# Kernel optimization log

Measured on AMD Instinct MI355X. Metric: run time of the kernel, lower is better.

## Reference

```python
import jax, jax.numpy as jnp
import numpy as np

B, T, F, D, HD = 16, 512, 16, 256, 256


def _init(k, shape, fan_in):
    return (jax.random.uniform(k, shape, minval=-1.0, maxval=1.0) / np.sqrt(fan_in)).astype(jnp.float32)


def setup_inputs() -> dict:
    key = jax.random.key(0)
    ks = jax.random.split(key, 16)
    return {
        "x": jax.random.normal(ks[0], (B, T, F), dtype=jnp.float32),
        # per-variable encoder params, batched over F (Linear(1,D) + GRN(D,HD,D))
        "w1": _init(ks[1], (F, D), 1), "b1": _init(ks[2], (F, D), 1),
        "fc1_w": _init(ks[3], (F, D, HD), D), "fc1_b": _init(ks[4], (F, HD), D),
        "fc2_w": _init(ks[5], (F, HD, D), HD), "fc2_b": _init(ks[6], (F, D), HD),
        "glu_w": _init(ks[7], (F, D, 2 * D), D), "glu_b": _init(ks[8], (F, 2 * D), D),
        "ln_g": jnp.ones((F, D), jnp.float32), "ln_b": jnp.zeros((F, D), jnp.float32),
        # weight GRN(F, HD, F); skip is Identity since d_in == d_out
        "wg_fc1_w": _init(ks[9], (F, HD), F), "wg_fc1_b": _init(ks[10], (HD,), F),
        "wg_fc2_w": _init(ks[11], (HD, F), HD), "wg_fc2_b": _init(ks[12], (F,), HD),
        "wg_glu_w": _init(ks[13], (F, 2 * F), F), "wg_glu_b": _init(ks[14], (2 * F,), F),
        "wg_ln_g": jnp.ones((F,), jnp.float32), "wg_ln_b": jnp.zeros((F,), jnp.float32),
    }


def _layernorm(x, g, b, eps=1e-5):
    m = jnp.mean(x, axis=-1, keepdims=True)
    v = jnp.var(x, axis=-1, keepdims=True)
    return (x - m) * jax.lax.rsqrt(v + eps) * g + b


def reference(x, w1, b1, fc1_w, fc1_b, fc2_w, fc2_b, glu_w, glu_b, ln_g, ln_b,
              wg_fc1_w, wg_fc1_b, wg_fc2_w, wg_fc2_b, wg_glu_w, wg_glu_b,
              wg_ln_g, wg_ln_b):
    # --- per-variable towers, batched over F (dropout is identity at eval) ---
    h0 = jax.nn.relu(x[..., None] * w1 + b1)                       # [B,T,F,D]
    y = jax.nn.elu(jnp.einsum('btfd,fdh->btfh', h0, fc1_w) + fc1_b)
    y = jnp.einsum('btfh,fhd->btfd', y, fc2_w) + fc2_b
    g = jnp.einsum('btfd,fde->btfe', y, glu_w) + glu_b             # [B,T,F,2D]
    a, gate = jnp.split(g, 2, axis=-1)
    H = _layernorm(h0 + a * jax.nn.sigmoid(gate), ln_g, ln_b)      # [B,T,F,D]
    # --- variable-weight GRN (time_distributed=True) ---
    yw = jax.nn.elu(x @ wg_fc1_w + wg_fc1_b)
    yw = yw @ wg_fc2_w + wg_fc2_b
    gw = x @ jnp.zeros((F, 0), x.dtype) if False else yw @ wg_glu_w + wg_glu_b
    aw, gatew = jnp.split(gw, 2, axis=-1)
    w = _layernorm(x + aw * jax.nn.sigmoid(gatew), wg_ln_g, wg_ln_b)
    w = jax.nn.softmax(w, axis=-1)                                 # [B,T,F]
    z = jnp.einsum('btfd,btf->btd', H, w)                          # [B,T,D]
    return z, w
```

## Files before the change

### kernel.cpp

```cpp
#include <hip/hip_runtime.h>
#include <hip/hip_bf16.h>

#define NBT 8192
#define NF  16
#define ND  256
#define NH  256
#define N2D 512

typedef short bf16x8 __attribute__((ext_vector_type(8)));
typedef float f32x4 __attribute__((ext_vector_type(4)));
typedef unsigned short u16x8 __attribute__((ext_vector_type(8)));

__device__ __forceinline__ float bf2f(unsigned short u) {
  return __uint_as_float(((unsigned)u) << 16);
}
__device__ __forceinline__ unsigned short f2bf(float f) {
  unsigned u = __float_as_uint(f);
  return (unsigned short)((u + 0x7FFFu + ((u >> 16) & 1u)) >> 16);
}

#define GLOAD16(src, dst)                                                     \
  __builtin_amdgcn_global_load_lds(                                           \
      (const __attribute__((address_space(1))) unsigned int*)(src),           \
      (__attribute__((address_space(3))) unsigned int*)(dst), 16, 0, 0)

__global__ __launch_bounds__(256) void wgrn_kernel(
    const float* __restrict__ x, const float* __restrict__ fw1,
    const float* __restrict__ fb1, const float* __restrict__ fw2,
    const float* __restrict__ fb2, const float* __restrict__ gwt,
    const float* __restrict__ gbt, const float* __restrict__ lng,
    const float* __restrict__ lnb, float* __restrict__ wout) {
  __shared__ float w1t[256 * 16];
  __shared__ float w2s[256 * 16];
  const int tid = threadIdx.x;
  for (int i = tid; i < 4096; i += 256) {
    int ff = i >> 8, j = i & 255;
    w1t[j * 16 + ff] = fw1[i];
    w2s[i] = fw2[i];
  }
  __syncthreads();
  const int sub  = tid & 7;
  const int rowi = tid >> 3;
  const int bt   = blockIdx.x * 32 + rowi;
  float xr[16];
#pragma unroll
  for (int i = 0; i < 4; ++i)
    *(float4*)&xr[i * 4] = *(const float4*)(x + (size_t)bt * 16 + i * 4);
  float acc2[16];
#pragma unroll
  for (int q = 0; q < 16; ++q) acc2[q] = 0.f;
  for (int j = sub; j < 256; j += 8) {
    float h = fb1[j];
    const float* wr = &w1t[j * 16];
#pragma unroll
    for (int q = 0; q < 16; ++q) h = fmaf(xr[q], wr[q], h);
    h = h > 0.f ? h : expm1f(h);
    const float* w2r = &w2s[j * 16];
#pragma unroll
    for (int q = 0; q < 16; ++q) acc2[q] = fmaf(h, w2r[q], acc2[q]);
  }
#pragma unroll
  for (int off = 1; off < 8; off <<= 1) {
#pragma unroll
    for (int q = 0; q < 16; ++q) acc2[q] += __shfl_xor(acc2[q], off);
  }
#pragma unroll
  for (int q = 0; q < 16; ++q) acc2[q] += fb2[q];
  float gw[32];
#pragma unroll
  for (int k = 0; k < 32; ++k) {
    float s = gbt[k];
#pragma unroll
    for (int q = 0; q < 16; ++q) s = fmaf(acc2[q], gwt[q * 32 + k], s);
    gw[k] = s;
  }
  float v[16];
  float mean = 0.f;
#pragma unroll
  for (int q = 0; q < 16; ++q) {
    float sg = 1.f / (1.f + __expf(-gw[16 + q]));
    v[q] = fmaf(gw[q], sg, xr[q]);
    mean += v[q];
  }
  mean *= (1.f / 16.f);
  float var = 0.f;
#pragma unroll
  for (int q = 0; q < 16; ++q) { float d = v[q] - mean; var = fmaf(d, d, var); }
  var *= (1.f / 16.f);
  float rstd = rsqrtf(var + 1e-5f);
  float mx = -1e30f;
#pragma unroll
  for (int q = 0; q < 16; ++q) {
    v[q] = (v[q] - mean) * rstd * lng[q] + lnb[q];
    mx = fmaxf(mx, v[q]);
  }
  float se = 0.f;
#pragma unroll
  for (int q = 0; q < 16; ++q) { v[q] = __expf(v[q] - mx); se += v[q]; }
  float inv = 1.f / se;
  if (sub == 0) {
#pragma unroll
    for (int i = 0; i < 4; ++i) {
      float4 o = { v[i*4+0]*inv, v[i*4+1]*inv, v[i*4+2]*inv, v[i*4+3]*inv };
      *(float4*)(wout + (size_t)bt * 16 + i * 4) = o;
    }
  }
}

__global__ void transpose_all(const float* __restrict__ fc1_w,
                              const float* __restrict__ fc2_w,
                              const float* __restrict__ glu_w,
                              unsigned short* __restrict__ fc1t,
                              unsigned short* __restrict__ fc2t,
                              unsigned short* __restrict__ glut) {
  __shared__ float tile[32][33];
  const int which = blockIdx.z >> 4;
  const int f     = blockIdx.z & 15;
  const float* src;
  unsigned short* dst;
  int K, N, bx = blockIdx.x;
  if (which == 0)      { src = fc1_w; dst = fc1t; K = ND; N = NH; }
  else if (which == 1) { src = fc2_w; dst = fc2t; K = NH; N = ND; }
  else                 { src = glu_w; dst = glut; K = ND; N = N2D;
                         bx += (which == 3) ? 8 : 0; }
  if (bx * 32 >= N) return;
  const float* s = src + (size_t)f * K * N;
  unsigned short* d = dst + (size_t)f * K * N;
  const int k0 = blockIdx.y * 32, n0 = bx * 32;
  const int tx = threadIdx.x, ty = threadIdx.y;
#pragma unroll
  for (int i = 0; i < 32; i += 8)
    tile[ty + i][tx] = s[(size_t)(k0 + ty + i) * N + n0 + tx];
  __syncthreads();
#pragma unroll
  for (int i = 0; i < 32; i += 8)
    d[(size_t)(n0 + ty + i) * K + k0 + tx] = f2bf(tile[tx][ty + i]);
}

__global__ __launch_bounds__(256, 4) void g1_kernel(
    const float* __restrict__ x, const float* __restrict__ w1,
    const float* __restrict__ b1, const unsigned short* __restrict__ fc1t,
    const float* __restrict__ fc1_b, unsigned short* __restrict__ y1) {
  __shared__ __align__(16) char arena[34816];
  __shared__ float xw[128];
  unsigned short* abuf = (unsigned short*)arena;
  unsigned short* bbuf = (unsigned short*)(arena + 17408);
  unsigned short* cbuf = (unsigned short*)arena;
  const int tid = threadIdx.x, lane = tid & 63, wid = tid >> 6;
  const int rl = lane & 15, kc = lane >> 4;
  int hb = blockIdx.x + 2 * (blockIdx.y + 64 * blockIdx.z);
  int L  = (hb & 7) * 256 + (hb >> 3);
  const int f = L >> 7, m0 = ((L >> 1) & 63) * 128, n0 = (L & 1) * 128;
  const unsigned short* Bf = fc1t + (size_t)f * NH * ND;
  const float* w1f = w1 + f * ND;
  const float* b1f = b1 + f * ND;
  if (tid < 128) xw[tid] = x[(size_t)(m0 + tid) * NF + f];
  const int wm = (wid >> 1) * 64, wn = (wid & 1) * 64;

  f32x4 acc[4][4];
#pragma unroll
  for (int m = 0; m < 4; ++m)
#pragma unroll
    for (int n = 0; n < 4; ++n) acc[m][n] = (f32x4){0.f, 0.f, 0.f, 0.f};

  for (int kt = 0; kt < ND; kt += 64) {
    __syncthreads();
#pragma unroll
    for (int i = 0; i < 4; ++i) {
      int s = tid + 256 * i;
      int row = s >> 3, sl = s & 7;
      const unsigned short* gb =
          Bf + (size_t)(n0 + row) * ND + kt + ((sl ^ (row & 7)) << 3);
      GLOAD16(gb, (char*)bbuf + (wid * 64 + 256 * i) * 16);
    }
#pragma unroll
    for (int i = 0; i < 4; ++i) {
      int vi = tid + 256 * i;
      int row = vi >> 3, c8 = vi & 7, c = kt + c8 * 8;
      float xv = xw[row];
      float4 wa = *(const float4*)(w1f + c);
      float4 wb = *(const float4*)(w1f + c + 4);
      float4 ba = *(const float4*)(b1f + c);
      float4 bb = *(const float4*)(b1f + c + 4);
      u16x8 o;
      o[0] = f2bf(fmaxf(fmaf(xv, wa.x, ba.x), 0.f));
      o[1] = f2bf(fmaxf(fmaf(xv, wa.y, ba.y), 0.f));
      o[2] = f2bf(fmaxf(fmaf(xv, wa.z, ba.z), 0.f));
      o[3] = f2bf(fmaxf(fmaf(xv, wa.w, ba.w), 0.f));
      o[4] = f2bf(fmaxf(fmaf(xv, wb.x, bb.x), 0.f));
      o[5] = f2bf(fmaxf(fmaf(xv, wb.y, bb.y), 0.f));
      o[6] = f2bf(fmaxf(fmaf(xv, wb.z, bb.z), 0.f));
      o[7] = f2bf(fmaxf(fmaf(xv, wb.w, bb.w), 0.f));
      *(u16x8*)(abuf + row * 68 + c8 * 8) = o;
    }
    __syncthreads();
#pragma unroll
    for (int kk = 0; kk < 2; ++kk) {
      bf16x8 av[4], bv[4];
      int s = kk * 4 + kc;
#pragma unroll
      for (int m = 0; m < 4; ++m) {
        int r = wm + m * 16 + rl;
        av[m] = *(const bf16x8*)(abuf + r * 68 + s * 8);
      }
#pragma unroll
      for (int n = 0; n < 4; ++n) {
        int rr = wn + n * 16 + rl;
        int ps = s ^ (rr & 7);
        bv[n] = *(const bf16x8*)((const char*)bbuf + rr * 128 + ps * 16);
      }
#pragma unroll
      for (int m = 0; m < 4; ++m)
#pragma unroll
        for (int n = 0; n < 4; ++n)
          acc[m][n] = __builtin_amdgcn_mfma_f32_16x16x32_bf16(av[m], bv[n],
                                                              acc[m][n], 0, 0, 0);
    }
  }

  __syncthreads();
  const int rq = lane >> 4;
#pragma unroll
  for (int n = 0; n < 4; ++n) {
    int cl = wn + n * 16 + rl;
    float bvv = fc1_b[f * NH + n0 + cl];
#pragma unroll
    for (int m = 0; m < 4; ++m) {
#pragma unroll
      for (int j = 0; j < 4; ++j) {
        int r = wm + m * 16 + rq * 4 + j;
        float v = acc[m][n][j] + bvv;
        v = v > 0.f ? v : expm1f(v);
        cbuf[r * 136 + cl] = f2bf(v);
      }
    }
  }
  __syncthreads();
#pragma unroll
  for (int v = 0; v < 8; ++v) {
    int row = (tid >> 4) + v * 16, chunk = tid & 15;
    u16x8 val = *(const u16x8*)(cbuf + row * 136 + chunk * 8);
    *(u16x8*)(y1 + ((size_t)f * NBT + m0 + row) * NH + n0 + chunk * 8) = val;
  }
}

__global__ __launch_bounds__(512, 4) void g2_kernel(
    const unsigned short* __restrict__ y1,
    const unsigned short* __restrict__ fc2t, const float* __restrict__ fc2_b,
    unsigned short* __restrict__ y2) {
  __shared__ __align__(16) char arena[49152];
  unsigned short* abuf = (unsigned short*)arena;
  unsigned short* bbuf = (unsigned short*)(arena + 16384);
  unsigned short* cbuf = (unsigned short*)arena;
  const int tid = threadIdx.x, lane = tid & 63, wid = tid >> 6;
  const int rl = lane & 15, kc = lane >> 4;
  int hb = blockIdx.x + 64 * blockIdx.y;
  int L  = (hb & 7) * 128 + (hb >> 3);
  const int f = L >> 6, m0 = (L & 63) * 128;
  const unsigned short* Af = y1 + (size_t)f * NBT * NH;
  const unsigned short* Bf = fc2t + (size_t)f * ND * NH;
  const int wm = (wid >> 2) * 64, wn = (wid & 3) * 64;

  f32x4 acc[4][4];
#pragma unroll
  for (int m = 0; m < 4; ++m)
#pragma unroll
    for (int n = 0; n < 4; ++n) acc[m][n] = (f32x4){0.f, 0.f, 0.f, 0.f};

  for (int kt = 0; kt < NH; kt += 64) {
    __syncthreads();
#pragma unroll
    for (int i = 0; i < 2; ++i) {
      int s = tid + 512 * i;
      int row = s >> 3, sl = s & 7;
      const unsigned short* ga =
          Af + (size_t)(m0 + row) * NH + kt + ((sl ^ (row & 7)) << 3);
      GLOAD16(ga, (char*)abuf + (wid * 64 + 512 * i) * 16);
    }
#pragma unroll
    for (int i = 0; i < 4; ++i) {
      int s = tid + 512 * i;
      int row = s >> 3, sl = s & 7;
      const unsigned short* gb =
          Bf + (size_t)row * NH + kt + ((sl ^ (row & 7)) << 3);
      GLOAD16(gb, (char*)bbuf + (wid * 64 + 512 * i) * 16);
    }
    __syncthreads();
#pragma unroll
    for (int kk = 0; kk < 2; ++kk) {
      bf16x8 av[4], bv[4];
      int s = kk * 4 + kc;
#pragma unroll
      for (int m = 0; m < 4; ++m) {
        int r = wm + m * 16 + rl;
        int ps = s ^ (r & 7);
        av[m] = *(const bf16x8*)((const char*)abuf + r * 128 + ps * 16);
      }
#pragma unroll
      for (int n = 0; n < 4; ++n) {
        int rr = wn + n * 16 + rl;
        int ps = s ^ (rr & 7);
        bv[n] = *(const bf16x8*)((const char*)bbuf + rr * 128 + ps * 16);
      }
#pragma unroll
      for (int m = 0; m < 4; ++m)
#pragma unroll
        for (int n = 0; n < 4; ++n)
          acc[m][n] = __builtin_amdgcn_mfma_f32_16x16x32_bf16(av[m], bv[n],
                                                              acc[m][n], 0, 0, 0);
    }
  }

  __syncthreads();
  const int rq = lane >> 4;
  const int hsel = (wid & 3) >> 1;
#pragma unroll
  for (int h = 0; h < 2; ++h) {
    if (h) __syncthreads();
    if (hsel == h) {
#pragma unroll
      for (int n = 0; n < 4; ++n) {
        int c = wn + n * 16 + rl;
        int cl = c - h * 128;
        float bvv = fc2_b[f * ND + c];
#pragma unroll
        for (int m = 0; m < 4; ++m) {
#pragma unroll
          for (int j = 0; j < 4; ++j) {
            int r = wm + m * 16 + rq * 4 + j;
            cbuf[r * 136 + cl] = f2bf(acc[m][n][j] + bvv);
          }
        }
      }
    }
    __syncthreads();
#pragma unroll
    for (int v = 0; v < 4; ++v) {
      int row = (tid >> 4) + v * 32, chunk = tid & 15;
      u16x8 val = *(const u16x8*)(cbuf + row * 136 + chunk * 8);
      *(u16x8*)(y2 + ((size_t)f * NBT + m0 + row) * ND + h * 128 + chunk * 8) =
          val;
    }
  }
}

__global__ __launch_bounds__(512, 4) void g3_kernel(
    const unsigned short* __restrict__ y2,
    const unsigned short* __restrict__ glut, const float* __restrict__ glu_b,
    const float* __restrict__ x, const float* __restrict__ w1,
    const float* __restrict__ b1, const float* __restrict__ ln_g,
    const float* __restrict__ ln_b, unsigned short* __restrict__ H) {
  __shared__ __align__(16) char arena[73728];
  __shared__ float xw[64];
  __shared__ float2 sums[8][64];
  __shared__ float2 sums2[64];
  unsigned short* abuf = (unsigned short*)arena;
  unsigned short* bbuf = (unsigned short*)(arena + 8192);
  unsigned short* vbuf = (unsigned short*)arena;

  const int tid = threadIdx.x, lane = tid & 63, wid = tid >> 6;
  const int rl = lane & 15, rq = lane >> 4;
  int hb = blockIdx.x + 128 * blockIdx.y;
  int L  = (hb & 7) * 256 + (hb >> 3);
  const int f = L >> 7, m0 = (L & 127) * 64;
  const unsigned short* Af = y2 + (size_t)f * NBT * ND;
  const unsigned short* Bf = glut + (size_t)f * ND * N2D;
  const float* w1f = w1 + f * ND;
  const float* b1f = b1 + f * ND;
  const int colb = wid * 32;
  if (tid < 64) xw[tid] = x[(size_t)(m0 + tid) * NF + f];

  f32x4 acc[4][4];
#pragma unroll
  for (int m = 0; m < 4; ++m)
#pragma unroll
    for (int n = 0; n < 4; ++n) acc[m][n] = (f32x4){0.f, 0.f, 0.f, 0.f};

  for (int kt = 0; kt < ND; kt += 64) {
    __syncthreads();
    {
      int s = tid;
      int row = s >> 3, sl = s & 7;
      const unsigned short* ga =
          Af + (size_t)(m0 + row) * ND + kt + ((sl ^ (row & 7)) << 3);
      GLOAD16(ga, (char*)abuf + (wid * 64) * 16);
    }
#pragma unroll
    for (int i = 0; i < 8; ++i) {
      int s = tid + 512 * i;
      int row = s >> 3, sl = s & 7;
      const unsigned short* gb =
          Bf + (size_t)row * ND + kt + ((sl ^ (row & 7)) << 3);
      GLOAD16(gb, (char*)bbuf + (wid * 64 + 512 * i) * 16);
    }
    __syncthreads();
#pragma unroll
    for (int kk = 0; kk < 2; ++kk) {
      bf16x8 av[4], bv[4];
      int s = kk * 4 + rq;
#pragma unroll
      for (int m = 0; m < 4; ++m) {
        int r = m * 16 + rl;
        int ps = s ^ (r & 7);
        av[m] = *(const bf16x8*)((const char*)abuf + r * 128 + ps * 16);
      }
#pragma unroll
      for (int n = 0; n < 4; ++n) {
        int rr = (n < 2) ? (colb + n * 16 + rl)
                         : (256 + colb + (n - 2) * 16 + rl);
        int ps = s ^ (rr & 7);
        bv[n] = *(const bf16x8*)((const char*)bbuf + rr * 128 + ps * 16);
      }
#pragma unroll
      for (int m = 0; m < 4; ++m)
#pragma unroll
        for (int n = 0; n < 4; ++n)
          acc[m][n] = __builtin_amdgcn_mfma_f32_16x16x32_bf16(av[m], bv[n],
                                                              acc[m][n], 0, 0, 0);
    }
  }

#pragma unroll
  for (int n = 0; n < 2; ++n) {
    int cA = colb + n * 16 + rl;
    float ab_ = glu_b[f * N2D + cA];
    float gb_ = glu_b[f * N2D + 256 + cA];
    float w1c = w1f[cA], b1c = b1f[cA];
#pragma unroll
    for (int m = 0; m < 4; ++m) {
#pragma unroll
      for (int j = 0; j < 4; ++j) {
        int r = m * 16 + rq * 4 + j;
        float a = acc[m][n][j] + ab_;
        float g = acc[m][n + 2][j] + gb_;
        float sg = 1.f / (1.f + __expf(-g));
        float h0 = fmaxf(fmaf(xw[r], w1c, b1c), 0.f);
        acc[m][n][j] = fmaf(a, sg, h0);
      }
    }
  }
#pragma unroll
  for (int m = 0; m < 4; ++m) {
#pragma unroll
    for (int j = 0; j < 4; ++j) {
      float s = acc[m][0][j] + acc[m][1][j];
      float q = fmaf(acc[m][0][j], acc[m][0][j],
                     acc[m][1][j] * acc[m][1][j]);
#pragma unroll
      for (int off = 1; off < 16; off <<= 1) {
        s += __shfl_xor(s, off);
        q += __shfl_xor(q, off);
      }
      if (rl == 0) sums[wid][m * 16 + rq * 4 + j] = make_float2(s, q);
    }
  }
  __syncthreads();
  if (tid < 64) {
    float tot = 0.f, tot2 = 0.f;
#pragma unroll
    for (int wv = 0; wv < 8; ++wv) {
      float2 p = sums[wv][tid];
      tot += p.x;
      tot2 += p.y;
    }
    float mean = tot * (1.f / 256.f);
    float var  = tot2 * (1.f / 256.f) - mean * mean;
    sums2[tid] = make_float2(mean, rsqrtf(var + 1e-5f));
  }
  __syncthreads();
#pragma unroll
  for (int n = 0; n < 2; ++n) {
    int cA = colb + n * 16 + rl;
    float lg = ln_g[f * ND + cA], lb = ln_b[f * ND + cA];
#pragma unroll
    for (int m = 0; m < 4; ++m) {
#pragma unroll
      for (int j = 0; j < 4; ++j) {
        int r = m * 16 + rq * 4 + j;
        float2 mr = sums2[r];
        vbuf[r * 264 + cA] = f2bf(fmaf((acc[m][n][j] - mr.x) * mr.y, lg, lb));
      }
    }
  }
  __syncthreads();
  {
    int row = tid >> 3, chunk = tid & 7;
    unsigned short* Hrow = H + ((size_t)f * NBT + m0 + row) * ND;
#pragma unroll
    for (int v = 0; v < 4; ++v) {
      u16x8 val = *(const u16x8*)(vbuf + row * 264 + chunk * 8 + v * 64);
      *(u16x8*)(Hrow + chunk * 8 + v * 64) = val;
    }
  }
}

__global__ __launch_bounds__(256) void combine_kernel(
    const unsigned short* __restrict__ H, const float* __restrict__ w,
    float* __restrict__ z) {
  int idx = blockIdx.x * 256 + threadIdx.x;
  int bt = idx >> 5;
  int d  = (idx & 31) << 3;
  float a[8];
#pragma unroll
  for (int j = 0; j < 8; ++j) a[j] = 0.f;
#pragma unroll
  for (int f = 0; f < 16; ++f) {
    u16x8 hv = *(const u16x8*)(H + ((size_t)f * NBT + bt) * ND + d);
    float wvv = w[bt * 16 + f];
#pragma unroll
    for (int j = 0; j < 8; ++j) a[j] = fmaf(bf2f(hv[j]), wvv, a[j]);
  }
  float4 o0 = {a[0], a[1], a[2], a[3]};
  float4 o1 = {a[4], a[5], a[6], a[7]};
  *(float4*)(z + (size_t)bt * ND + d)     = o0;
  *(float4*)(z + (size_t)bt * ND + d + 4) = o1;
}

extern "C" void kernel_launch(void* const* d_in, const int* in_sizes, int n_in,
                              void* d_out, int out_size, void* d_ws,
                              size_t ws_size, hipStream_t stream) {
  const float* x        = (const float*)d_in[0];
  const float* w1       = (const float*)d_in[1];
  const float* b1       = (const float*)d_in[2];
  const float* fc1_w    = (const float*)d_in[3];
  const float* fc1_b    = (const float*)d_in[4];
  const float* fc2_w    = (const float*)d_in[5];
  const float* fc2_b    = (const float*)d_in[6];
  const float* glu_w    = (const float*)d_in[7];
  const float* glu_b    = (const float*)d_in[8];
  const float* ln_g     = (const float*)d_in[9];
  const float* ln_b     = (const float*)d_in[10];
  const float* wg_fc1_w = (const float*)d_in[11];
  const float* wg_fc1_b = (const float*)d_in[12];
  const float* wg_fc2_w = (const float*)d_in[13];
  const float* wg_fc2_b = (const float*)d_in[14];
  const float* wg_glu_w = (const float*)d_in[15];
  const float* wg_glu_b = (const float*)d_in[16];
  const float* wg_ln_g  = (const float*)d_in[17];
  const float* wg_ln_b  = (const float*)d_in[18];

  char* ws = (char*)d_ws;
  unsigned short* fc1t = (unsigned short*)ws;
  unsigned short* fc2t = fc1t + (size_t)NF * NH * ND;
  unsigned short* glut = fc2t + (size_t)NF * ND * NH;
  unsigned short* y1   = (unsigned short*)(ws + (8ull << 20));
  unsigned short* y2   = (unsigned short*)(ws + (72ull << 20));
  unsigned short* Hbuf = (unsigned short*)(ws + (136ull << 20));

  float* zout = (float*)d_out;
  float* wout = zout + (size_t)NBT * ND;

  wgrn_kernel<<<256, 256, 0, stream>>>(x, wg_fc1_w, wg_fc1_b, wg_fc2_w,
                                       wg_fc2_b, wg_glu_w, wg_glu_b, wg_ln_g,
                                       wg_ln_b, wout);
  transpose_all<<<dim3(16, 8, 64), dim3(32, 8), 0, stream>>>(
      fc1_w, fc2_w, glu_w, fc1t, fc2t, glut);

  g1_kernel<<<dim3(NH / 128, NBT / 128, NF), 256, 0, stream>>>(
      x, w1, b1, fc1t, fc1_b, y1);
  g2_kernel<<<dim3(NBT / 128, NF), 512, 0, stream>>>(y1, fc2t, fc2_b, y2);
  g3_kernel<<<dim3(NBT / 64, NF), 512, 0, stream>>>(y2, glut, glu_b, x, w1, b1,
                                                    ln_g, ln_b, Hbuf);
  combine_kernel<<<(NBT * ND / 8) / 256, 256, 0, stream>>>(Hbuf, wout, zout);

  (void)in_sizes; (void)n_in; (void)out_size; (void)ws_size;
}
```

Measured before the change: 227.0 us.

## Fuse fc1 and fc2 GEMMs into one kernel keeping intermediate in LDS

Merges the first two per-variable GEMMs into a single kernel. Each block computes a 64-row tile of h0, runs fc1 with ELU into shared memory, then runs fc2 from that shared tile, so the y1 intermediate never goes to global memory. This removes a 64 MB bf16 write plus its read-back and one kernel launch. In exchange the tiles are smaller (64 rows, 32 columns per wave), with fewer MFMAs per B-tile load, a larger LDS footprint and lower occupancy per CU.

Measured after the change: 195.5 us, median of 2. 13.9% less time.

```diff
diff --git a/kernel.cpp b/kernel.cpp
--- a/kernel.cpp
+++ b/kernel.cpp
@@ -137,210 +137,164 @@
     d[(size_t)(n0 + ty + i) * K + k0 + tx] = f2bf(tile[tx][ty + i]);
 }
 
-__global__ __launch_bounds__(256, 4) void g1_kernel(
+__global__ __launch_bounds__(512, 2) void g12_kernel(
     const float* __restrict__ x, const float* __restrict__ w1,
     const float* __restrict__ b1, const unsigned short* __restrict__ fc1t,
-    const float* __restrict__ fc1_b, unsigned short* __restrict__ y1) {
-  __shared__ __align__(16) char arena[34816];
-  __shared__ float xw[128];
-  unsigned short* abuf = (unsigned short*)arena;
-  unsigned short* bbuf = (unsigned short*)(arena + 17408);
-  unsigned short* cbuf = (unsigned short*)arena;
+    const float* __restrict__ fc1_b, const unsigned short* __restrict__ fc2t,
+    const float* __restrict__ fc2_b, unsigned short* __restrict__ y2) {
+  __shared__ __align__(16) unsigned short hbuf[64 * 264];
+  __shared__ __align__(16) unsigned short bstg[256 * 64];
+  __shared__ float xw[64];
   const int tid = threadIdx.x, lane = tid & 63, wid = tid >> 6;
   const int rl = lane & 15, kc = lane >> 4;
-  int hb = blockIdx.x + 2 * (blockIdx.y + 64 * blockIdx.z);
+  int hb = blockIdx.x + 128 * blockIdx.y;
   int L  = (hb & 7) * 256 + (hb >> 3);
-  const int f = L >> 7, m0 = ((L >> 1) & 63) * 128, n0 = (L & 1) * 128;
-  const unsigned short* Bf = fc1t + (size_t)f * NH * ND;
+  const int f = L >> 7, m0 = (L & 127) * 64;
+  const unsigned short* B1 = fc1t + (size_t)f * NH * ND;
+  const unsigned short* B2 = fc2t + (size_t)f * ND * NH;
   const float* w1f = w1 + f * ND;
   const float* b1f = b1 + f * ND;
-  if (tid < 128) xw[tid] = x[(size_t)(m0 + tid) * NF + f];
-  const int wm = (wid >> 1) * 64, wn = (wid & 1) * 64;
-
-  f32x4 acc[4][4];
+  const int wn = wid * 32;
+
+  if (tid < 64) xw[tid] = x[(size_t)(m0 + tid) * NF + f];
+  __syncthreads();
+
+#pragma unroll
+  for (int i = 0; i < 4; ++i) {
+    int j = tid + 512 * i;
+    int row = j >> 5, c = (j & 31) * 8;
+    float xv = xw[row];
+    float4 wa = *(const float4*)(w1f + c);
+    float4 wb = *(const float4*)(w1f + c + 4);
+    float4 ba = *(const float4*)(b1f + c);
+    float4 bb = *(const float4*)(b1f + c + 4);
+    u16x8 o;
+    o[0] = f2bf(fmaxf(fmaf(xv, wa.x, ba.x), 0.f));
+    o[1] = f2bf(fmaxf(fmaf(xv, wa.y, ba.y), 0.f));
+    o[2] = f2bf(fmaxf(fmaf(xv, wa.z, ba.z), 0.f));
+    o[3] = f2bf(fmaxf(fmaf(xv, wa.w, ba.w), 0.f));
+    o[4] = f2bf(fmaxf(fmaf(xv, wb.x, bb.x), 0.f));
+    o[5] = f2bf(fmaxf(fmaf(xv, wb.y, bb.y), 0.f));
+    o[6] = f2bf(fmaxf(fmaf(xv, wb.z, bb.z), 0.f));
+    o[7] = f2bf(fmaxf(fmaf(xv, wb.w, bb.w), 0.f));
+    *(u16x8*)(hbuf + row * 264 + c) = o;
+  }
+  __syncthreads();
+
+  f32x4 acc[4][2];
 #pragma unroll
   for (int m = 0; m < 4; ++m)
 #pragma unroll
-    for (int n = 0; n < 4; ++n) acc[m][n] = (f32x4){0.f, 0.f, 0.f, 0.f};
+    for (int n = 0; n < 2; ++n) acc[m][n] = (f32x4){0.f, 0.f, 0.f, 0.f};
 
   for (int kt = 0; kt < ND; kt += 64) {
-    __syncthreads();
-#pragma unroll
-    for (int i = 0; i < 4; ++i) {
-      int s = tid + 256 * i;
-      int row = s >> 3, sl = s & 7;
-      const unsigned short* gb =
-          Bf + (size_t)(n0 + row) * ND + kt + ((sl ^ (row & 7)) << 3);
-      GLOAD16(gb, (char*)bbuf + (wid * 64 + 256 * i) * 16);
-    }
-#pragma unroll
-    for (int i = 0; i < 4; ++i) {
-      int vi = tid + 256 * i;
-      int row = vi >> 3, c8 = vi & 7, c = kt + c8 * 8;
-      float xv = xw[row];
-      float4 wa = *(const float4*)(w1f + c);
-      float4 wb = *(const float4*)(w1f + c + 4);
-      float4 ba = *(const float4*)(b1f + c);
-      float4 bb = *(const float4*)(b1f + c + 4);
-      u16x8 o;
-      o[0] = f2bf(fmaxf(fmaf(xv, wa.x, ba.x), 0.f));
-      o[1] = f2bf(fmaxf(fmaf(xv, wa.y, ba.y), 0.f));
-      o[2] = f2bf(fmaxf(fmaf(xv, wa.z, ba.z), 0.f));
-      o[3] = f2bf(fmaxf(fmaf(xv, wa.w, ba.w), 0.f));
-      o[4] = f2bf(fmaxf(fmaf(xv, wb.x, bb.x), 0.f));
-      o[5] = f2bf(fmaxf(fmaf(xv, wb.y, bb.y), 0.f));
-      o[6] = f2bf(fmaxf(fmaf(xv, wb.z, bb.z), 0.f));
-      o[7] = f2bf(fmaxf(fmaf(xv, wb.w, bb.w), 0.f));
-      *(u16x8*)(abuf + row * 68 + c8 * 8) = o;
-    }
-    __syncthreads();
-#pragma unroll
-    for (int kk = 0; kk < 2; ++kk) {
-      bf16x8 av[4], bv[4];
-      int s = kk * 4 + kc;
-#pragma unroll
-      for (int m = 0; m < 4; ++m) {
-        int r = wm + m * 16 + rl;
-        av[m] = *(const bf16x8*)(abuf + r * 68 + s * 8);
-      }
-#pragma unroll
-      for (int n = 0; n < 4; ++n) {
-        int rr = wn + n * 16 + rl;
-        int ps = s ^ (rr & 7);
-        bv[n] = *(const bf16x8*)((const char*)bbuf + rr * 128 + ps * 16);
-      }
-#pragma unroll
-      for (int m = 0; m < 4; ++m)
-#pragma unroll
-        for (int n = 0; n < 4; ++n)
-          acc[m][n] = __builtin_amdgcn_mfma_f32_16x16x32_bf16(av[m], bv[n],
-                                                              acc[m][n], 0, 0, 0);
-    }
-  }
-
-  __syncthreads();
-  const int rq = lane >> 4;
-#pragma unroll
-  for (int n = 0; n < 4; ++n) {
-    int cl = wn + n * 16 + rl;
-    float bvv = fc1_b[f * NH + n0 + cl];
-#pragma unroll
-    for (int m = 0; m < 4; ++m) {
-#pragma unroll
-      for (int j = 0; j < 4; ++j) {
-        int r = wm + m * 16 + rq * 4 + j;
-        float v = acc[m][n][j] + bvv;
-        v = v > 0.f ? v : expm1f(v);
-        cbuf[r * 136 + cl] = f2bf(v);
-      }
-    }
-  }
-  __syncthreads();
-#pragma unroll
-  for (int v = 0; v < 8; ++v) {
-    int row = (tid >> 4) + v * 16, chunk = tid & 15;
-    u16x8 val = *(const u16x8*)(cbuf + row * 136 + chunk * 8);
-    *(u16x8*)(y1 + ((size_t)f * NBT + m0 + row) * NH + n0 + chunk * 8) = val;
-  }
-}
-
-__global__ __launch_bounds__(512, 4) void g2_kernel(
-    const unsigned short* __restrict__ y1,
-    const unsigned short* __restrict__ fc2t, const float* __restrict__ fc2_b,
-    unsigned short* __restrict__ y2) {
-  __shared__ __align__(16) char arena[49152];
-  unsigned short* abuf = (unsigned short*)arena;
-  unsigned short* bbuf = (unsigned short*)(arena + 16384);
-  unsigned short* cbuf = (unsigned short*)arena;
-  const int tid = threadIdx.x, lane = tid & 63, wid = tid >> 6;
-  const int rl = lane & 15, kc = lane >> 4;
-  int hb = blockIdx.x + 64 * blockIdx.y;
-  int L  = (hb & 7) * 128 + (hb >> 3);
-  const int f = L >> 6, m0 = (L & 63) * 128;
-  const unsigned short* Af = y1 + (size_t)f * NBT * NH;
-  const unsigned short* Bf = fc2t + (size_t)f * ND * NH;
-  const int wm = (wid >> 2) * 64, wn = (wid & 3) * 64;
-
-  f32x4 acc[4][4];
-#pragma unroll
-  for (int m = 0; m < 4; ++m)
-#pragma unroll
-    for (int n = 0; n < 4; ++n) acc[m][n] = (f32x4){0.f, 0.f, 0.f, 0.f};
-
-  for (int kt = 0; kt < NH; kt += 64) {
-    __syncthreads();
-#pragma unroll
-    for (int i = 0; i < 2; ++i) {
-      int s = tid + 512 * i;
-      int row = s >> 3, sl = s & 7;
-      const unsigned short* ga =
-          Af + (size_t)(m0 + row) * NH + kt + ((sl ^ (row & 7)) << 3);
-      GLOAD16(ga, (char*)abuf + (wid * 64 + 512 * i) * 16);
-    }
+    if (kt) __syncthreads();
 #pragma unroll
     for (int i = 0; i < 4; ++i) {
       int s = tid + 512 * i;
       int row = s >> 3, sl = s & 7;
-      const unsigned short* gb =
-          Bf + (size_t)row * NH + kt + ((sl ^ (row & 7)) << 3);
-      GLOAD16(gb, (char*)bbuf + (wid * 64 + 512 * i) * 16);
+      GLOAD16(B1 + (size_t)row * ND + kt + ((sl ^ (row & 7)) << 3),
+              (char*)bstg + (wid * 64 + 512 * i) * 16);
     }
     __syncthreads();
 #pragma unroll
     for (int kk = 0; kk < 2; ++kk) {
-      bf16x8 av[4], bv[4];
       int s = kk * 4 + kc;
-#pragma unroll
-      for (int m = 0; m < 4; ++m) {
-        int r = wm + m * 16 + rl;
-        int ps = s ^ (r & 7);
-        av[m] = *(const bf16x8*)((const char*)abuf + r * 128 + ps * 16);
-      }
-#pragma unroll
-      for (int n = 0; n < 4; ++n) {
+      bf16x8 av[4], bv[2];
+#pragma unroll
+      for (int n = 0; n < 2; ++n) {
         int rr = wn + n * 16 + rl;
         int ps = s ^ (rr & 7);
-        bv[n] = *(const bf16x8*)((const char*)bbuf + rr * 128 + ps * 16);
+        bv[n] = *(const bf16x8*)((const char*)bstg + rr * 128 + ps * 16);
       }
 #pragma unroll
       for (int m = 0; m < 4; ++m)
-#pragma unroll
-        for (int n = 0; n < 4; ++n)
+        av[m] = *(const bf16x8*)(hbuf + (m * 16 + rl) * 264 + kt + s * 8);
+#pragma unroll
+      for (int m = 0; m < 4; ++m)
+#pragma unroll
+        for (int n = 0; n < 2; ++n)
           acc[m][n] = __builtin_amdgcn_mfma_f32_16x16x32_bf16(av[m], bv[n],
                                                               acc[m][n], 0, 0, 0);
     }
   }
-
-  __syncthreads();
-  const int rq = lane >> 4;
-  const int hsel = (wid & 3) >> 1;
-#pragma unroll
-  for (int h = 0; h < 2; ++h) {
-    if (h) __syncthreads();
-    if (hsel == h) {
-#pragma unroll
-      for (int n = 0; n < 4; ++n) {
-        int c = wn + n * 16 + rl;
-        int cl = c - h * 128;
-        float bvv = fc2_b[f * ND + c];
-#pragma unroll
-        for (int m = 0; m < 4; ++m) {
-#pragma unroll
-          for (int j = 0; j < 4; ++j) {
-            int r = wm + m * 16 + rq * 4 + j;
-            cbuf[r * 136 + cl] = f2bf(acc[m][n][j] + bvv);
-          }
-        }
-      }
+  __syncthreads();
+
+#pragma unroll
+  for (int n = 0; n < 2; ++n) {
+    int c = wn + n * 16 + rl;
+    float bvv = fc1_b[f * NH + c];
+#pragma unroll
+    for (int m = 0; m < 4; ++m) {
+#pragma unroll
+      for (int j = 0; j < 4; ++j) {
+        int r = m * 16 + kc * 4 + j;
+        float v = acc[m][n][j] + bvv;
+        v = v > 0.f ? v : expm1f(v);
+        hbuf[r * 264 + c] = f2bf(v);
+      }
+    }
+  }
+  __syncthreads();
+
+#pragma unroll
+  for (int m = 0; m < 4; ++m)
+#pragma unroll
+    for (int n = 0; n < 2; ++n) acc[m][n] = (f32x4){0.f, 0.f, 0.f, 0.f};
+
+  for (int kt = 0; kt < NH; kt += 64) {
+    if (kt) __syncthreads();
+#pragma unroll
+    for (int i = 0; i < 4; ++i) {
+      int s = tid + 512 * i;
+      int row = s >> 3, sl = s & 7;
+      GLOAD16(B2 + (size_t)row * NH + kt + ((sl ^ (row & 7)) << 3),
+              (char*)bstg + (wid * 64 + 512 * i) * 16);
     }
     __syncthreads();
 #pragma unroll
-    for (int v = 0; v < 4; ++v) {
-      int row = (tid >> 4) + v * 32, chunk = tid & 15;
-      u16x8 val = *(const u16x8*)(cbuf + row * 136 + chunk * 8);
-      *(u16x8*)(y2 + ((size_t)f * NBT + m0 + row) * ND + h * 128 + chunk * 8) =
-          val;
-    }
+    for (int kk = 0; kk < 2; ++kk) {
+      int s = kk * 4 + kc;
+      bf16x8 av[4], bv[2];
+#pragma unroll
+      for (int n = 0; n < 2; ++n) {
+        int rr = wn + n * 16 + rl;
+        int ps = s ^ (rr & 7);
+        bv[n] = *(const bf16x8*)((const char*)bstg + rr * 128 + ps * 16);
+      }
+#pragma unroll
+      for (int m = 0; m < 4; ++m)
+        av[m] = *(const bf16x8*)(hbuf + (m * 16 + rl) * 264 + kt + s * 8);
+#pragma unroll
+      for (int m = 0; m < 4; ++m)
+#pragma unroll
+        for (int n = 0; n < 2; ++n)
+          acc[m][n] = __builtin_amdgcn_mfma_f32_16x16x32_bf16(av[m], bv[n],
+                                                              acc[m][n], 0, 0, 0);
+    }
+  }
+  __syncthreads();
+
+#pragma unroll
+  for (int n = 0; n < 2; ++n) {
+    int c = wn + n * 16 + rl;
+    float bvv = fc2_b[f * ND + c];
+#pragma unroll
+    for (int m = 0; m < 4; ++m) {
+#pragma unroll
+      for (int j = 0; j < 4; ++j) {
+        int r = m * 16 + kc * 4 + j;
+        hbuf[r * 264 + c] = f2bf(acc[m][n][j] + bvv);
+      }
+    }
+  }
+  __syncthreads();
+#pragma unroll
+  for (int v = 0; v < 4; ++v) {
+    int job = tid + 512 * v;
+    int row = job >> 5, ch = job & 31;
+    u16x8 val = *(const u16x8*)(hbuf + row * 264 + ch * 8);
+    *(u16x8*)(y2 + ((size_t)f * NBT + m0 + row) * ND + ch * 8) = val;
   }
 }
 
@@ -543,9 +497,8 @@
   unsigned short* fc1t = (unsigned short*)ws;
   unsigned short* fc2t = fc1t + (size_t)NF * NH * ND;
   unsigned short* glut = fc2t + (size_t)NF * ND * NH;
-  unsigned short* y1   = (unsigned short*)(ws + (8ull << 20));
-  unsigned short* y2   = (unsigned short*)(ws + (72ull << 20));
-  unsigned short* Hbuf = (unsigned short*)(ws + (136ull << 20));
+  unsigned short* y2   = (unsigned short*)(ws + (8ull << 20));
+  unsigned short* Hbuf = (unsigned short*)(ws + (72ull << 20));
 
   float* zout = (float*)d_out;
   float* wout = zout + (size_t)NBT * ND;
@@ -556,11 +509,10 @@
   transpose_all<<<dim3(16, 8, 64), dim3(32, 8), 0, stream>>>(
       fc1_w, fc2_w, glu_w, fc1t, fc2t, glut);
 
-  g1_kernel<<<dim3(NH / 128, NBT / 128, NF), 256, 0, stream>>>(
-      x, w1, b1, fc1t, fc1_b, y1);
-  g2_kernel<<<dim3(NBT / 128, NF), 512, 0, stream>>>(y1, fc2t, fc2_b, y2);
-  g3_kernel<<<dim3(NBT / 64, NF), 512, 0, stream>>>(y2, glut, glu_b, x, w1, b1,
-                                                    ln_g, ln_b, Hbuf);
+  g12_kernel<<<dim3(128, 16), 512, 0, stream>>>(x, w1, b1, fc1t, fc1_b, fc2t,
+                                                fc2_b, y2);
+  g3_kernel<<<dim3(128, 16), 512, 0, stream>>>(y2, glut, glu_b, x, w1, b1,
+                                               ln_g, ln_b, Hbuf);
   combine_kernel<<<(NBT * ND / 8) / 256, 256, 0, stream>>>(Hbuf, wout, zout);
 
   (void)in_sizes; (void)n_in; (void)out_size; (void)ws_size;
```
